# Performance work log

Measured on AMD Instinct MI355X. Metric: run time of the kernel, lower is better.

The kernel has to match this reference:

```python
import jax, jax.numpy as jnp
import numpy as np

D_MODEL = 1024
N_HEAD = 16
D_K = D_MODEL // N_HEAD
SEQ_LEN = 2048
BATCH = 2
NEG = -1e8


def setup_inputs() -> dict:
    key = jax.random.key(0)
    ks = jax.random.split(key, 8)
    scale = 1.0 / np.sqrt(D_MODEL)
    inp = {
        "input": jax.random.normal(ks[0], (BATCH, SEQ_LEN, D_MODEL), dtype=jnp.float32),
        "mask": jax.random.randint(ks[1], (BATCH, SEQ_LEN), 0, 2) == 1,  # True = masked
        "Wq": jax.random.uniform(ks[2], (D_MODEL, D_MODEL), jnp.float32, -scale, scale),
        "bq": jax.random.uniform(ks[3], (D_MODEL,), jnp.float32, -scale, scale),
        "Wk": jax.random.uniform(ks[4], (D_MODEL, D_MODEL), jnp.float32, -scale, scale),
        "bk": jax.random.uniform(ks[5], (D_MODEL,), jnp.float32, -scale, scale),
        "Wv": jax.random.uniform(ks[6], (D_MODEL, D_MODEL), jnp.float32, -scale, scale),
        "bv": jax.random.uniform(ks[7], (D_MODEL,), jnp.float32, -scale, scale),
    }
    return inp


def reference(input, mask, Wq, bq, Wk, bk, Wv, bv):
    B, S, D = input.shape
    # nn.Linear: y = x @ W^T + b
    def split_heads(x):
        return x.reshape(B, S, N_HEAD, D_K).transpose(0, 2, 1, 3)  # [B,H,S,d_k]

    Q = split_heads(input @ Wq.T + bq)
    K = split_heads(input @ Wk.T + bk)
    V = split_heads(input @ Wv.T + bv)

    scores = jnp.einsum('bhqd,bhkd->bhqk', Q, K) / jnp.sqrt(jnp.float32(D_K))
    # mask [B,S] broadcast over heads and query positions (key mask)
    scores = jnp.where(mask[:, None, None, :], NEG, scores)
    attn = jax.nn.softmax(scores, axis=-1)
    out = jnp.einsum('bhqk,bhkd->bhqd', attn, V)  # [B,H,S,d_k]
    return out.transpose(0, 2, 1, 3).reshape(B, S, D)
```

## Files before the change

kernel.cpp:

```cpp
#include <hip/hip_runtime.h>
#include <math.h>

#define D_MODEL 1024
#define NH 16
#define DK 64
#define SEQ 2048
#define BATCH 2
#define MTOT (BATCH * SEQ)

typedef unsigned short u16;
typedef unsigned int u32;
typedef short bf16x8 __attribute__((ext_vector_type(8)));
typedef short bf16x4 __attribute__((ext_vector_type(4)));
typedef float f32x4 __attribute__((ext_vector_type(4)));

static constexpr float NEGV = -1e8f;

__device__ __forceinline__ u16 f2bf(float f) {
    union { float f; u32 u; } v; v.f = f;
    u32 r = v.u + 0x7FFFu + ((v.u >> 16) & 1u);
    return (u16)(r >> 16);
}

__device__ __forceinline__ f32x4 mfma16(bf16x4 a, bf16x4 b, f32x4 c) {
#if __has_builtin(__builtin_amdgcn_mfma_f32_16x16x16_bf16)
    return __builtin_amdgcn_mfma_f32_16x16x16_bf16(a, b, c, 0, 0, 0);
#else
    return __builtin_amdgcn_mfma_f32_16x16x16bf16_1k(a, b, c, 0, 0, 0);
#endif
}

__device__ __forceinline__ void stage16(const u16* g, u16* lds_per_lane) {
#if __has_builtin(__builtin_amdgcn_global_load_lds)
    __builtin_amdgcn_global_load_lds((const __attribute__((address_space(1))) u32*)g,
                                     (__attribute__((address_space(3))) u32*)lds_per_lane,
                                     16, 0, 0);
#else
    *(uint4*)lds_per_lane = *(const uint4*)g;
#endif
}

__global__ __launch_bounds__(256) void convert_bf16(
    const float* __restrict__ X, const float* __restrict__ Wq,
    const float* __restrict__ Wk, const float* __restrict__ Wv,
    u16* __restrict__ Xb, u16* __restrict__ Wb)
{
    const int NX = MTOT * D_MODEL / 4;
    const int NW = D_MODEL * D_MODEL / 4;
    int i = blockIdx.x * 256 + threadIdx.x;
    if (i >= NX + 3 * NW) return;
    float4 v; u16* dst;
    if (i < NX)             { v = ((const float4*)X )[i];            dst = Xb + (size_t)i * 4; }
    else if (i < NX + NW)   { v = ((const float4*)Wq)[i - NX];       dst = Wb + (size_t)(i - NX) * 4; }
    else if (i < NX + 2*NW) { v = ((const float4*)Wk)[i - NX - NW];  dst = Wb + (size_t)NW * 4 + (size_t)(i - NX - NW) * 4; }
    else                    { v = ((const float4*)Wv)[i - NX - 2*NW];dst = Wb + (size_t)NW * 8 + (size_t)(i - NX - 2*NW) * 4; }
    ushort4 o;
    o.x = f2bf(v.x); o.y = f2bf(v.y); o.z = f2bf(v.z); o.w = f2bf(v.w);
    *(ushort4*)dst = o;
}

__global__ __launch_bounds__(256, 2) void proj_mfma(
    const u16* __restrict__ Xb, const u16* __restrict__ Wb,
    const float* __restrict__ bq, const float* __restrict__ bk, const float* __restrict__ bv,
    u16* __restrict__ Qb, u16* __restrict__ Kb, u16* __restrict__ Vb)
{
    __shared__ u16 As[128 * 32];
    __shared__ u16 Bs[128 * 32];

    const int which = blockIdx.z;
    const u16* __restrict__ W = Wb + (size_t)which * D_MODEL * D_MODEL;
    const float* __restrict__ bias = which == 0 ? bq : (which == 1 ? bk : bv);
    u16* __restrict__ Out = which == 0 ? Qb : (which == 1 ? Kb : Vb);

    const int m0 = blockIdx.x * 128, n0 = blockIdx.y * 128;
    const int tid = threadIdx.x, lane = tid & 63, w = tid >> 6;
    const int quad = lane >> 4, l15 = lane & 15;
    const int wr = w >> 1, wc = w & 1;

    f32x4 acc[4][4];
#pragma unroll
    for (int i = 0; i < 4; i++)
#pragma unroll
        for (int j = 0; j < 4; j++) acc[i][j] = (f32x4)0.0f;

    const int srow = 32 * w + (lane >> 2);
    const int scol = (lane & 3) * 8;

    for (int k0 = 0; k0 < D_MODEL; k0 += 32) {
#pragma unroll
        for (int t = 0; t < 2; t++) {
            stage16(Xb + (size_t)(m0 + srow + 16 * t) * D_MODEL + k0 + scol,
                    &As[(32 * w + 16 * t) * 32 + lane * 8]);
            stage16(W + (size_t)(n0 + srow + 16 * t) * D_MODEL + k0 + scol,
                    &Bs[(32 * w + 16 * t) * 32 + lane * 8]);
        }
        __syncthreads();
        bf16x8 af[4], bfr[4];
#pragma unroll
        for (int i = 0; i < 4; i++)
            af[i] = *(const bf16x8*)&As[(wr * 64 + i * 16 + l15) * 32 + quad * 8];
#pragma unroll
        for (int j = 0; j < 4; j++)
            bfr[j] = *(const bf16x8*)&Bs[(wc * 64 + j * 16 + l15) * 32 + quad * 8];
#pragma unroll
        for (int i = 0; i < 4; i++)
#pragma unroll
            for (int j = 0; j < 4; j++)
                acc[i][j] = __builtin_amdgcn_mfma_f32_16x16x32_bf16(af[i], bfr[j], acc[i][j], 0, 0, 0);
        __syncthreads();
    }

    float bj[4];
#pragma unroll
    for (int j = 0; j < 4; j++) bj[j] = bias[n0 + wc * 64 + j * 16 + l15];
#pragma unroll
    for (int i = 0; i < 4; i++) {
#pragma unroll
        for (int j = 0; j < 4; j++) {
#pragma unroll
            for (int r = 0; r < 4; r++) {
                int m = m0 + wr * 64 + i * 16 + quad * 4 + r;
                int n = n0 + wc * 64 + j * 16 + l15;
                int b = m >> 11, s = m & (SEQ - 1);
                int h = n >> 6, d = n & 63;
                Out[(((size_t)b * NH + h) * SEQ + s) * DK + d] = f2bf(acc[i][j][r] + bj[j]);
            }
        }
    }
}

__global__ __launch_bounds__(256, 2) void attn_mfma(
    const u16* __restrict__ Qg, const u16* __restrict__ Kg, const u16* __restrict__ Vg,
    const int* __restrict__ mask, float* __restrict__ out)
{
    constexpr int PADK = 72, PADV = 72;
    __shared__ u16 Ks[2][64 * PADK];
    __shared__ u16 Vt[2][64 * PADV];
    __shared__ float mads[SEQ];

    const int qt0 = blockIdx.x, h = blockIdx.y, b = blockIdx.z;
    const int tid = threadIdx.x, lane = tid & 63, w = tid >> 6;
    const int quad = lane >> 4, l15 = lane & 15;
    const size_t bh = (size_t)b * NH + h;
    const u16* __restrict__ Qp = Qg + (bh * SEQ + qt0 * 128) * DK;
    const u16* __restrict__ Kp = Kg + bh * SEQ * DK;
    const u16* __restrict__ Vp = Vg + bh * SEQ * DK;
    const int* __restrict__ mp = mask + b * SEQ;

    for (int i = tid; i < SEQ; i += 256) mads[i] = mp[i] ? NEGV : 0.0f;

    const int q0 = w * 32;
    bf16x8 qf[2][2];
#pragma unroll
    for (int qt = 0; qt < 2; qt++)
#pragma unroll
        for (int half = 0; half < 2; half++)
            qf[qt][half] = *(const bf16x8*)(Qp + (size_t)(q0 + qt * 16 + l15) * DK + half * 32 + quad * 8);

    const int skey = tid & 63, sdk = (tid >> 6) * 16;
    const int vkp2 = (tid & 31) * 2, vd0 = (tid >> 5) * 8;

    {
        const u16* kr = Kp + (size_t)skey * DK + sdk;
        bf16x8 k0 = *(const bf16x8*)kr, k1 = *(const bf16x8*)(kr + 8);
        u16* kd = &Ks[0][skey * PADK + sdk];
        *(bf16x8*)kd = k0; *(bf16x8*)(kd + 8) = k1;
        const u16* vr = Vp + (size_t)vkp2 * DK + vd0;
        bf16x8 v0 = *(const bf16x8*)vr, v1 = *(const bf16x8*)(vr + DK);
#pragma unroll
        for (int i = 0; i < 8; i++)
            *(u32*)&Vt[0][(vd0 + i) * PADV + vkp2] = (u32)(u16)v0[i] | ((u32)(u16)v1[i] << 16);
    }
    __syncthreads();

    f32x4 O[4][2];
    float mrow[2], lrow[2];
#pragma unroll
    for (int dt = 0; dt < 4; dt++)
#pragma unroll
        for (int qt = 0; qt < 2; qt++) O[dt][qt] = (f32x4)0.0f;
    mrow[0] = mrow[1] = -__builtin_huge_valf();
    lrow[0] = lrow[1] = 0.0f;

    for (int kt = 0; kt < SEQ / 64; kt++) {
        const int bb = kt & 1;
        bf16x8 nk0, nk1, nv0, nv1;
        if (kt < SEQ / 64 - 1) {
            const u16* kr = Kp + (size_t)((kt + 1) * 64 + skey) * DK + sdk;
            nk0 = *(const bf16x8*)kr; nk1 = *(const bf16x8*)(kr + 8);
            const u16* vr = Vp + (size_t)((kt + 1) * 64 + vkp2) * DK + vd0;
            nv0 = *(const bf16x8*)vr; nv1 = *(const bf16x8*)(vr + DK);
        }

        f32x4 St[4][2];
#pragma unroll
        for (int ktl = 0; ktl < 4; ktl++) {
            bf16x8 kf0 = *(const bf16x8*)&Ks[bb][(ktl * 16 + l15) * PADK + quad * 8];
            bf16x8 kf1 = *(const bf16x8*)&Ks[bb][(ktl * 16 + l15) * PADK + 32 + quad * 8];
#pragma unroll
            for (int qt = 0; qt < 2; qt++) {
                f32x4 acc = (f32x4)0.0f;
                acc = __builtin_amdgcn_mfma_f32_16x16x32_bf16(kf0, qf[qt][0], acc, 0, 0, 0);
                acc = __builtin_amdgcn_mfma_f32_16x16x32_bf16(kf1, qf[qt][1], acc, 0, 0, 0);
                St[ktl][qt] = acc;
            }
        }

#pragma unroll
        for (int ktl = 0; ktl < 4; ktl++) {
            f32x4 ma = *(const f32x4*)&mads[kt * 64 + ktl * 16 + quad * 4];
#pragma unroll
            for (int qt = 0; qt < 2; qt++)
#pragma unroll
                for (int r = 0; r < 4; r++)
                    St[ktl][qt][r] = St[ktl][qt][r] * 0.125f + ma[r];
        }

        float alpha[2];
#pragma unroll
        for (int qt = 0; qt < 2; qt++) {
            float mx = St[0][qt][0];
#pragma unroll
            for (int ktl = 0; ktl < 4; ktl++)
#pragma unroll
                for (int r = 0; r < 4; r++) mx = fmaxf(mx, St[ktl][qt][r]);
            mx = fmaxf(mx, __shfl_xor(mx, 16));
            mx = fmaxf(mx, __shfl_xor(mx, 32));
            float mn = fmaxf(mrow[qt], mx);
            alpha[qt] = __expf(mrow[qt] - mn);
            mrow[qt] = mn;
            float sum = 0.0f;
#pragma unroll
            for (int ktl = 0; ktl < 4; ktl++)
#pragma unroll
                for (int r = 0; r < 4; r++) {
                    float p = __expf(St[ktl][qt][r] - mn);
                    St[ktl][qt][r] = p;
                    sum += p;
                }
            sum += __shfl_xor(sum, 16);
            sum += __shfl_xor(sum, 32);
            lrow[qt] = alpha[qt] * lrow[qt] + sum;
        }

        bf16x4 pf[4][2];
#pragma unroll
        for (int ktl = 0; ktl < 4; ktl++)
#pragma unroll
            for (int qt = 0; qt < 2; qt++) {
                bf16x4 pp;
#pragma unroll
                for (int r = 0; r < 4; r++) pp[r] = (short)f2bf(St[ktl][qt][r]);
                pf[ktl][qt] = pp;
            }

#pragma unroll
        for (int dt = 0; dt < 4; dt++)
#pragma unroll
            for (int qt = 0; qt < 2; qt++)
#pragma unroll
                for (int r = 0; r < 4; r++) O[dt][qt][r] *= alpha[qt];

#pragma unroll
        for (int ktl = 0; ktl < 4; ktl++)
#pragma unroll
            for (int dt = 0; dt < 4; dt++) {
                bf16x4 vf = *(const bf16x4*)&Vt[bb][(dt * 16 + l15) * PADV + ktl * 16 + quad * 4];
#pragma unroll
                for (int qt = 0; qt < 2; qt++)
                    O[dt][qt] = mfma16(vf, pf[ktl][qt], O[dt][qt]);
            }

        if (kt < SEQ / 64 - 1) {
            u16* kd = &Ks[bb ^ 1][skey * PADK + sdk];
            *(bf16x8*)kd = nk0; *(bf16x8*)(kd + 8) = nk1;
#pragma unroll
            for (int i = 0; i < 8; i++)
                *(u32*)&Vt[bb ^ 1][(vd0 + i) * PADV + vkp2] = (u32)(u16)nv0[i] | ((u32)(u16)nv1[i] << 16);
        }
        __syncthreads();
    }

    float inv[2] = {1.0f / lrow[0], 1.0f / lrow[1]};
#pragma unroll
    for (int qt = 0; qt < 2; qt++) {
        int q = qt0 * 128 + q0 + qt * 16 + l15;
        float* op = out + ((size_t)b * SEQ + q) * D_MODEL + h * DK;
#pragma unroll
        for (int dt = 0; dt < 4; dt++)
#pragma unroll
            for (int r = 0; r < 4; r++)
                op[dt * 16 + quad * 4 + r] = O[dt][qt][r] * inv[qt];
    }
}

extern "C" void kernel_launch(void* const* d_in, const int* in_sizes, int n_in,
                              void* d_out, int out_size, void* d_ws, size_t ws_size,
                              hipStream_t stream)
{
    const float* X  = (const float*)d_in[0];
    const int* mask = (const int*)d_in[1];
    const float* Wq = (const float*)d_in[2];
    const float* bq = (const float*)d_in[3];
    const float* Wk = (const float*)d_in[4];
    const float* bk = (const float*)d_in[5];
    const float* Wv = (const float*)d_in[6];
    const float* bv = (const float*)d_in[7];
    float* out = (float*)d_out;

    u16* Xb = (u16*)d_ws;
    u16* Wb = Xb + (size_t)MTOT * D_MODEL;
    u16* Qb = Wb + (size_t)3 * D_MODEL * D_MODEL;
    u16* Kb = Qb + (size_t)BATCH * NH * SEQ * DK;
    u16* Vb = Kb + (size_t)BATCH * NH * SEQ * DK;

    const int ncvt = (MTOT * D_MODEL + 3 * D_MODEL * D_MODEL) / 4;
    convert_bf16<<<(ncvt + 255) / 256, 256, 0, stream>>>(X, Wq, Wk, Wv, Xb, Wb);
    proj_mfma<<<dim3(MTOT / 128, D_MODEL / 128, 3), 256, 0, stream>>>(Xb, Wb, bq, bk, bv, Qb, Kb, Vb);
    attn_mfma<<<dim3(SEQ / 128, NH, BATCH), 256, 0, stream>>>(Qb, Kb, Vb, mask, out);
}
```

Before: 185.8 us.

## Write transposed V from projection, drop LDS staging in attention, use exp2 softmax

The projection kernel now writes V pre-transposed (head, d, seq) and swaps the MFMA operands for Q/K so it can emit vectorized ushort4 stores. The attention kernel drops its shared-memory staging and barriers. Each wave loads K fragments and transposed-V fragments straight from global memory, double-buffering K in registers. The softmax folds log2(e) into the scale so it can use exp2, and the mask-to-additive conversion moves into the convert kernel. Together these aim to cut LDS traffic, syncs and scalar stores. The cost is redundant global/L2 reads of K and V across the four waves of each block, plus higher register pressure.

```diff
diff --git a/kernel.cpp b/kernel.cpp
--- a/kernel.cpp
+++ b/kernel.cpp
@@ -1,4 +1,5 @@
 #include <hip/hip_runtime.h>
+#include <hip/hip_bf16.h>
 #include <math.h>
 
 #define D_MODEL 1024
@@ -7,6 +8,7 @@
 #define SEQ 2048
 #define BATCH 2
 #define MTOT (BATCH * SEQ)
+#define NC (SEQ / 64)
 
 typedef unsigned short u16;
 typedef unsigned int u32;
@@ -14,12 +16,22 @@
 typedef short bf16x4 __attribute__((ext_vector_type(4)));
 typedef float f32x4 __attribute__((ext_vector_type(4)));
 
-static constexpr float NEGV = -1e8f;
-
-__device__ __forceinline__ u16 f2bf(float f) {
-    union { float f; u32 u; } v; v.f = f;
-    u32 r = v.u + 0x7FFFu + ((v.u >> 16) & 1u);
-    return (u16)(r >> 16);
+static constexpr float SCALE_LOG2 = 0.18033688011112042f;
+static constexpr float MASKADD = -1.0e9f;
+
+__device__ __forceinline__ u32 pk2(float a, float b) {
+    __hip_bfloat162 t = __float22bfloat162_rn(float2{a, b});
+    return *(u32*)&t;
+}
+__device__ __forceinline__ ushort4 pk4u(float a, float b, float c, float d) {
+    union { ushort4 s4; u32 w[2]; } u;
+    u.w[0] = pk2(a, b); u.w[1] = pk2(c, d);
+    return u.s4;
+}
+__device__ __forceinline__ bf16x4 pk4b(float a, float b, float c, float d) {
+    union { bf16x4 v; u32 w[2]; } u;
+    u.w[0] = pk2(a, b); u.w[1] = pk2(c, d);
+    return u.v;
 }
 
 __device__ __forceinline__ f32x4 mfma16(bf16x4 a, bf16x4 b, f32x4 c) {
@@ -43,26 +55,35 @@
 __global__ __launch_bounds__(256) void convert_bf16(
     const float* __restrict__ X, const float* __restrict__ Wq,
     const float* __restrict__ Wk, const float* __restrict__ Wv,
-    u16* __restrict__ Xb, u16* __restrict__ Wb)
+    const int* __restrict__ mask,
+    u16* __restrict__ Xb, u16* __restrict__ Wb, float* __restrict__ madsg)
 {
     const int NX = MTOT * D_MODEL / 4;
     const int NW = D_MODEL * D_MODEL / 4;
+    const int NM = MTOT / 4;
     int i = blockIdx.x * 256 + threadIdx.x;
-    if (i >= NX + 3 * NW) return;
+    if (i >= NX + 3 * NW + NM) return;
+    if (i >= NX + 3 * NW) {
+        int j = i - NX - 3 * NW;
+        int4 m = ((const int4*)mask)[j];
+        float4 o;
+        o.x = m.x ? MASKADD : 0.0f; o.y = m.y ? MASKADD : 0.0f;
+        o.z = m.z ? MASKADD : 0.0f; o.w = m.w ? MASKADD : 0.0f;
+        ((float4*)madsg)[j] = o;
+        return;
+    }
     float4 v; u16* dst;
     if (i < NX)             { v = ((const float4*)X )[i];            dst = Xb + (size_t)i * 4; }
     else if (i < NX + NW)   { v = ((const float4*)Wq)[i - NX];       dst = Wb + (size_t)(i - NX) * 4; }
     else if (i < NX + 2*NW) { v = ((const float4*)Wk)[i - NX - NW];  dst = Wb + (size_t)NW * 4 + (size_t)(i - NX - NW) * 4; }
     else                    { v = ((const float4*)Wv)[i - NX - 2*NW];dst = Wb + (size_t)NW * 8 + (size_t)(i - NX - 2*NW) * 4; }
-    ushort4 o;
-    o.x = f2bf(v.x); o.y = f2bf(v.y); o.z = f2bf(v.z); o.w = f2bf(v.w);
-    *(ushort4*)dst = o;
+    *(ushort4*)dst = pk4u(v.x, v.y, v.z, v.w);
 }
 
 __global__ __launch_bounds__(256, 2) void proj_mfma(
     const u16* __restrict__ Xb, const u16* __restrict__ Wb,
     const float* __restrict__ bq, const float* __restrict__ bk, const float* __restrict__ bv,
-    u16* __restrict__ Qb, u16* __restrict__ Kb, u16* __restrict__ Vb)
+    u16* __restrict__ Qb, u16* __restrict__ Kb, u16* __restrict__ Vtb)
 {
     __shared__ u16 As[128 * 32];
     __shared__ u16 Bs[128 * 32];
@@ -70,7 +91,6 @@
     const int which = blockIdx.z;
     const u16* __restrict__ W = Wb + (size_t)which * D_MODEL * D_MODEL;
     const float* __restrict__ bias = which == 0 ? bq : (which == 1 ? bk : bv);
-    u16* __restrict__ Out = which == 0 ? Qb : (which == 1 ? Kb : Vb);
 
     const int m0 = blockIdx.x * 128, n0 = blockIdx.y * 128;
     const int tid = threadIdx.x, lane = tid & 63, w = tid >> 6;
@@ -102,76 +122,80 @@
 #pragma unroll
         for (int j = 0; j < 4; j++)
             bfr[j] = *(const bf16x8*)&Bs[(wc * 64 + j * 16 + l15) * 32 + quad * 8];
-#pragma unroll
-        for (int i = 0; i < 4; i++)
-#pragma unroll
-            for (int j = 0; j < 4; j++)
-                acc[i][j] = __builtin_amdgcn_mfma_f32_16x16x32_bf16(af[i], bfr[j], acc[i][j], 0, 0, 0);
+        if (which < 2) {
+#pragma unroll
+            for (int i = 0; i < 4; i++)
+#pragma unroll
+                for (int j = 0; j < 4; j++)
+                    acc[i][j] = __builtin_amdgcn_mfma_f32_16x16x32_bf16(bfr[j], af[i], acc[i][j], 0, 0, 0);
+        } else {
+#pragma unroll
+            for (int i = 0; i < 4; i++)
+#pragma unroll
+                for (int j = 0; j < 4; j++)
+                    acc[i][j] = __builtin_amdgcn_mfma_f32_16x16x32_bf16(af[i], bfr[j], acc[i][j], 0, 0, 0);
+        }
         __syncthreads();
     }
 
-    float bj[4];
-#pragma unroll
-    for (int j = 0; j < 4; j++) bj[j] = bias[n0 + wc * 64 + j * 16 + l15];
-#pragma unroll
-    for (int i = 0; i < 4; i++) {
-#pragma unroll
-        for (int j = 0; j < 4; j++) {
-#pragma unroll
-            for (int r = 0; r < 4; r++) {
-                int m = m0 + wr * 64 + i * 16 + quad * 4 + r;
-                int n = n0 + wc * 64 + j * 16 + l15;
-                int b = m >> 11, s = m & (SEQ - 1);
-                int h = n >> 6, d = n & 63;
-                Out[(((size_t)b * NH + h) * SEQ + s) * DK + d] = f2bf(acc[i][j][r] + bj[j]);
+    if (which < 2) {
+        u16* __restrict__ Out = which == 0 ? Qb : Kb;
+        float4 bj4[4];
+#pragma unroll
+        for (int j = 0; j < 4; j++)
+            bj4[j] = *(const float4*)&bias[n0 + wc * 64 + j * 16 + quad * 4];
+#pragma unroll
+        for (int i = 0; i < 4; i++) {
+            int mcol = m0 + wr * 64 + i * 16 + l15;
+            int b_ = mcol >> 11, s = mcol & (SEQ - 1);
+#pragma unroll
+            for (int j = 0; j < 4; j++) {
+                int nrow = n0 + wc * 64 + j * 16 + quad * 4;
+                int hh = nrow >> 6, d = nrow & 63;
+                *(ushort4*)(Out + (((size_t)b_ * NH + hh) * SEQ + s) * DK + d) =
+                    pk4u(acc[i][j][0] + bj4[j].x, acc[i][j][1] + bj4[j].y,
+                         acc[i][j][2] + bj4[j].z, acc[i][j][3] + bj4[j].w);
             }
         }
+    } else {
+        float bjv[4];
+#pragma unroll
+        for (int j = 0; j < 4; j++) bjv[j] = bias[n0 + wc * 64 + j * 16 + l15];
+#pragma unroll
+        for (int i = 0; i < 4; i++) {
+            int srw = m0 + wr * 64 + i * 16 + quad * 4;
+            int b_ = srw >> 11, s = srw & (SEQ - 1);
+#pragma unroll
+            for (int j = 0; j < 4; j++) {
+                int ncol = n0 + wc * 64 + j * 16 + l15;
+                int hh = ncol >> 6, d = ncol & 63;
+                *(ushort4*)(Vtb + (((size_t)b_ * NH + hh) * DK + d) * SEQ + s) =
+                    pk4u(acc[i][j][0] + bjv[j], acc[i][j][1] + bjv[j],
+                         acc[i][j][2] + bjv[j], acc[i][j][3] + bjv[j]);
+            }
+        }
     }
 }
 
 __global__ __launch_bounds__(256, 2) void attn_mfma(
-    const u16* __restrict__ Qg, const u16* __restrict__ Kg, const u16* __restrict__ Vg,
-    const int* __restrict__ mask, float* __restrict__ out)
+    const u16* __restrict__ Qg, const u16* __restrict__ Kg, const u16* __restrict__ Vtg,
+    const float* __restrict__ madsg, float* __restrict__ out)
 {
-    constexpr int PADK = 72, PADV = 72;
-    __shared__ u16 Ks[2][64 * PADK];
-    __shared__ u16 Vt[2][64 * PADV];
-    __shared__ float mads[SEQ];
-
     const int qt0 = blockIdx.x, h = blockIdx.y, b = blockIdx.z;
     const int tid = threadIdx.x, lane = tid & 63, w = tid >> 6;
     const int quad = lane >> 4, l15 = lane & 15;
     const size_t bh = (size_t)b * NH + h;
-    const u16* __restrict__ Qp = Qg + (bh * SEQ + qt0 * 128) * DK;
+    const u16* __restrict__ Qp = Qg + (bh * SEQ + qt0 * 128 + w * 32) * DK;
     const u16* __restrict__ Kp = Kg + bh * SEQ * DK;
-    const u16* __restrict__ Vp = Vg + bh * SEQ * DK;
-    const int* __restrict__ mp = mask + b * SEQ;
-
-    for (int i = tid; i < SEQ; i += 256) mads[i] = mp[i] ? NEGV : 0.0f;
-
-    const int q0 = w * 32;
+    const u16* __restrict__ Vp = Vtg + bh * DK * SEQ;
+    const float* __restrict__ mp = madsg + b * SEQ;
+
     bf16x8 qf[2][2];
 #pragma unroll
     for (int qt = 0; qt < 2; qt++)
 #pragma unroll
         for (int half = 0; half < 2; half++)
-            qf[qt][half] = *(const bf16x8*)(Qp + (size_t)(q0 + qt * 16 + l15) * DK + half * 32 + quad * 8);
-
-    const int skey = tid & 63, sdk = (tid >> 6) * 16;
-    const int vkp2 = (tid & 31) * 2, vd0 = (tid >> 5) * 8;
-
-    {
-        const u16* kr = Kp + (size_t)skey * DK + sdk;
-        bf16x8 k0 = *(const bf16x8*)kr, k1 = *(const bf16x8*)(kr + 8);
-        u16* kd = &Ks[0][skey * PADK + sdk];
-        *(bf16x8*)kd = k0; *(bf16x8*)(kd + 8) = k1;
-        const u16* vr = Vp + (size_t)vkp2 * DK + vd0;
-        bf16x8 v0 = *(const bf16x8*)vr, v1 = *(const bf16x8*)(vr + DK);
-#pragma unroll
-        for (int i = 0; i < 8; i++)
-            *(u32*)&Vt[0][(vd0 + i) * PADV + vkp2] = (u32)(u16)v0[i] | ((u32)(u16)v1[i] << 16);
-    }
-    __syncthreads();
+            qf[qt][half] = *(const bf16x8*)(Qp + (size_t)(qt * 16 + l15) * DK + half * 32 + quad * 8);
 
     f32x4 O[4][2];
     float mrow[2], lrow[2];
@@ -182,39 +206,50 @@
     mrow[0] = mrow[1] = -__builtin_huge_valf();
     lrow[0] = lrow[1] = 0.0f;
 
-    for (int kt = 0; kt < SEQ / 64; kt++) {
-        const int bb = kt & 1;
-        bf16x8 nk0, nk1, nv0, nv1;
-        if (kt < SEQ / 64 - 1) {
-            const u16* kr = Kp + (size_t)((kt + 1) * 64 + skey) * DK + sdk;
-            nk0 = *(const bf16x8*)kr; nk1 = *(const bf16x8*)(kr + 8);
-            const u16* vr = Vp + (size_t)((kt + 1) * 64 + vkp2) * DK + vd0;
-            nv0 = *(const bf16x8*)vr; nv1 = *(const bf16x8*)(vr + DK);
-        }
+    bf16x8 kfA[4][2], kfB[4][2];
+#pragma unroll
+    for (int ktl = 0; ktl < 4; ktl++)
+#pragma unroll
+        for (int half = 0; half < 2; half++)
+            kfA[ktl][half] = *(const bf16x8*)(Kp + (size_t)(ktl * 16 + l15) * DK + half * 32 + quad * 8);
+
+    auto body = [&](int kt, bf16x8 (&kc)[4][2], bf16x8 (&kn)[4][2]) {
+        bf16x4 vf[4][4];
+#pragma unroll
+        for (int dt = 0; dt < 4; dt++)
+#pragma unroll
+            for (int ktl = 0; ktl < 4; ktl++)
+                vf[dt][ktl] = *(const bf16x4*)(Vp + (size_t)(dt * 16 + l15) * SEQ + kt * 64 + ktl * 16 + quad * 4);
+        f32x4 mav[4];
+#pragma unroll
+        for (int ktl = 0; ktl < 4; ktl++)
+            mav[ktl] = *(const f32x4*)(mp + kt * 64 + ktl * 16 + quad * 4);
+        int ktn = kt + 1; ktn = (ktn == NC) ? 0 : ktn;
+        const u16* kbase = Kp + (size_t)ktn * 64 * DK;
+#pragma unroll
+        for (int ktl = 0; ktl < 4; ktl++)
+#pragma unroll
+            for (int half = 0; half < 2; half++)
+                kn[ktl][half] = *(const bf16x8*)(kbase + (size_t)(ktl * 16 + l15) * DK + half * 32 + quad * 8);
 
         f32x4 St[4][2];
 #pragma unroll
-        for (int ktl = 0; ktl < 4; ktl++) {
-            bf16x8 kf0 = *(const bf16x8*)&Ks[bb][(ktl * 16 + l15) * PADK + quad * 8];
-            bf16x8 kf1 = *(const bf16x8*)&Ks[bb][(ktl * 16 + l15) * PADK + 32 + quad * 8];
+        for (int ktl = 0; ktl < 4; ktl++)
 #pragma unroll
             for (int qt = 0; qt < 2; qt++) {
                 f32x4 acc = (f32x4)0.0f;
-                acc = __builtin_amdgcn_mfma_f32_16x16x32_bf16(kf0, qf[qt][0], acc, 0, 0, 0);
-                acc = __builtin_amdgcn_mfma_f32_16x16x32_bf16(kf1, qf[qt][1], acc, 0, 0, 0);
+                acc = __builtin_amdgcn_mfma_f32_16x16x32_bf16(kc[ktl][0], qf[qt][0], acc, 0, 0, 0);
+                acc = __builtin_amdgcn_mfma_f32_16x16x32_bf16(kc[ktl][1], qf[qt][1], acc, 0, 0, 0);
                 St[ktl][qt] = acc;
             }
-        }
-
-#pragma unroll
-        for (int ktl = 0; ktl < 4; ktl++) {
-            f32x4 ma = *(const f32x4*)&mads[kt * 64 + ktl * 16 + quad * 4];
+
+#pragma unroll
+        for (int ktl = 0; ktl < 4; ktl++)
 #pragma unroll
             for (int qt = 0; qt < 2; qt++)
 #pragma unroll
                 for (int r = 0; r < 4; r++)
-                    St[ktl][qt][r] = St[ktl][qt][r] * 0.125f + ma[r];
-        }
+                    St[ktl][qt][r] = St[ktl][qt][r] * SCALE_LOG2 + mav[ktl][r];
 
         float alpha[2];
 #pragma unroll
@@ -227,14 +262,14 @@
             mx = fmaxf(mx, __shfl_xor(mx, 16));
             mx = fmaxf(mx, __shfl_xor(mx, 32));
             float mn = fmaxf(mrow[qt], mx);
-            alpha[qt] = __expf(mrow[qt] - mn);
+            alpha[qt] = exp2f(mrow[qt] - mn);
             mrow[qt] = mn;
             float sum = 0.0f;
 #pragma unroll
             for (int ktl = 0; ktl < 4; ktl++)
 #pragma unroll
                 for (int r = 0; r < 4; r++) {
-                    float p = __expf(St[ktl][qt][r] - mn);
+                    float p = exp2f(St[ktl][qt][r] - mn);
                     St[ktl][qt][r] = p;
                     sum += p;
                 }
@@ -247,12 +282,8 @@
 #pragma unroll
         for (int ktl = 0; ktl < 4; ktl++)
 #pragma unroll
-            for (int qt = 0; qt < 2; qt++) {
-                bf16x4 pp;
-#pragma unroll
-                for (int r = 0; r < 4; r++) pp[r] = (short)f2bf(St[ktl][qt][r]);
-                pf[ktl][qt] = pp;
-            }
+            for (int qt = 0; qt < 2; qt++)
+                pf[ktl][qt] = pk4b(St[ktl][qt][0], St[ktl][qt][1], St[ktl][qt][2], St[ktl][qt][3]);
 
 #pragma unroll
         for (int dt = 0; dt < 4; dt++)
@@ -264,33 +295,29 @@
 #pragma unroll
         for (int ktl = 0; ktl < 4; ktl++)
 #pragma unroll
-            for (int dt = 0; dt < 4; dt++) {
-                bf16x4 vf = *(const bf16x4*)&Vt[bb][(dt * 16 + l15) * PADV + ktl * 16 + quad * 4];
+            for (int dt = 0; dt < 4; dt++)
 #pragma unroll
                 for (int qt = 0; qt < 2; qt++)
-                    O[dt][qt] = mfma16(vf, pf[ktl][qt], O[dt][qt]);
-            }
-
-        if (kt < SEQ / 64 - 1) {
-            u16* kd = &Ks[bb ^ 1][skey * PADK + sdk];
-            *(bf16x8*)kd = nk0; *(bf16x8*)(kd + 8) = nk1;
-#pragma unroll
-            for (int i = 0; i < 8; i++)
-                *(u32*)&Vt[bb ^ 1][(vd0 + i) * PADV + vkp2] = (u32)(u16)nv0[i] | ((u32)(u16)nv1[i] << 16);
-        }
-        __syncthreads();
+                    O[dt][qt] = mfma16(vf[dt][ktl], pf[ktl][qt], O[dt][qt]);
+    };
+
+    for (int kt = 0; kt < NC; kt += 2) {
+        body(kt, kfA, kfB);
+        body(kt + 1, kfB, kfA);
     }
 
     float inv[2] = {1.0f / lrow[0], 1.0f / lrow[1]};
 #pragma unroll
     for (int qt = 0; qt < 2; qt++) {
-        int q = qt0 * 128 + q0 + qt * 16 + l15;
+        int q = qt0 * 128 + w * 32 + qt * 16 + l15;
         float* op = out + ((size_t)b * SEQ + q) * D_MODEL + h * DK;
 #pragma unroll
-        for (int dt = 0; dt < 4; dt++)
-#pragma unroll
-            for (int r = 0; r < 4; r++)
-                op[dt * 16 + quad * 4 + r] = O[dt][qt][r] * inv[qt];
+        for (int dt = 0; dt < 4; dt++) {
+            float4 o;
+            o.x = O[dt][qt][0] * inv[qt]; o.y = O[dt][qt][1] * inv[qt];
+            o.z = O[dt][qt][2] * inv[qt]; o.w = O[dt][qt][3] * inv[qt];
+            *(float4*)(op + dt * 16 + quad * 4) = o;
+        }
     }
 }
 
@@ -308,14 +335,15 @@
     const float* bv = (const float*)d_in[7];
     float* out = (float*)d_out;
 
-    u16* Xb = (u16*)d_ws;
-    u16* Wb = Xb + (size_t)MTOT * D_MODEL;
-    u16* Qb = Wb + (size_t)3 * D_MODEL * D_MODEL;
-    u16* Kb = Qb + (size_t)BATCH * NH * SEQ * DK;
-    u16* Vb = Kb + (size_t)BATCH * NH * SEQ * DK;
-
-    const int ncvt = (MTOT * D_MODEL + 3 * D_MODEL * D_MODEL) / 4;
-    convert_bf16<<<(ncvt + 255) / 256, 256, 0, stream>>>(X, Wq, Wk, Wv, Xb, Wb);
-    proj_mfma<<<dim3(MTOT / 128, D_MODEL / 128, 3), 256, 0, stream>>>(Xb, Wb, bq, bk, bv, Qb, Kb, Vb);
-    attn_mfma<<<dim3(SEQ / 128, NH, BATCH), 256, 0, stream>>>(Qb, Kb, Vb, mask, out);
-}
+    u16* Xb  = (u16*)d_ws;
+    u16* Wb  = Xb + (size_t)MTOT * D_MODEL;
+    u16* Qb  = Wb + (size_t)3 * D_MODEL * D_MODEL;
+    u16* Kb  = Qb + (size_t)BATCH * NH * SEQ * DK;
+    u16* Vtb = Kb + (size_t)BATCH * NH * SEQ * DK;
+    float* madsg = (float*)(Vtb + (size_t)BATCH * NH * SEQ * DK);
+
+    const int ncvt = MTOT * D_MODEL / 4 + 3 * D_MODEL * D_MODEL / 4 + MTOT / 4;
+    convert_bf16<<<(ncvt + 255) / 256, 256, 0, stream>>>(X, Wq, Wk, Wv, mask, Xb, Wb, madsg);
+    proj_mfma<<<dim3(MTOT / 128, D_MODEL / 128, 3), 256, 0, stream>>>(Xb, Wb, bq, bk, bv, Qb, Kb, Vtb);
+    attn_mfma<<<dim3(SEQ / 128, NH, BATCH), 256, 0, stream>>>(Qb, Kb, Vtb, madsg, out);
+}
```

New measurement: 325.2 us. 1.75x slower.
